# Kernel optimization log

Measured on AMD Instinct MI355X. Metric: run time of the kernel, lower is better.

## Reference

```python
import jax, jax.numpy as jnp
import numpy as np
import math

B, T, D = 2, 2048, 4096
H, HD = 32, 128  # n_head, head_dim; H*HD == D
THETA = 10000.0


def _rope_tables(T, hd, theta):
    # standard RoPE: freqs_i = theta^(-2i/hd), angle[t,i] = t * freqs_i
    inv = 1.0 / (theta ** (np.arange(0, hd, 2, dtype=np.float32) / hd))  # [hd/2]
    ang = np.arange(T, dtype=np.float32)[:, None] * inv[None, :]          # [T, hd/2]
    return jnp.asarray(np.cos(ang)), jnp.asarray(np.sin(ang))


def setup_inputs() -> dict:
    key = jax.random.key(0)
    ks = jax.random.split(key, 5)
    scale = 1.0 / math.sqrt(D)
    x = jax.random.normal(ks[0], (B, T, D), dtype=jnp.float32)
    Wq = jax.random.normal(ks[1], (D, H * HD), dtype=jnp.float32) * scale
    Wk = jax.random.normal(ks[2], (D, H * HD), dtype=jnp.float32) * scale
    Wv = jax.random.normal(ks[3], (D, H * HD), dtype=jnp.float32) * scale
    Wo = jax.random.normal(ks[4], (D, D), dtype=jnp.float32) * scale
    fc, fs = _rope_tables(T, HD, THETA)
    return {"x": x, "freqs_cos": fc, "freqs_sin": fs,
            "Wq": Wq, "Wk": Wk, "Wv": Wv, "Wo": Wo}


def _apply_rope(t, cos, sin):
    # t: [B, T, H, HD]; complex rotation on interleaved (even, odd) pairs
    tp = t.reshape(*t.shape[:-1], HD // 2, 2)
    xr, xi = tp[..., 0], tp[..., 1]
    c = cos[None, :, None, :]  # [1, T, 1, HD/2]
    s = sin[None, :, None, :]
    out_r = xr * c - xi * s
    out_i = xr * s + xi * c
    return jnp.stack([out_r, out_i], axis=-1).reshape(t.shape)


def reference(x, freqs_cos, freqs_sin, Wq, Wk, Wv, Wo):
    Bc, Tc, _ = x.shape
    q = (x @ Wq).reshape(Bc, Tc, H, HD)
    k = (x @ Wk).reshape(Bc, Tc, H, HD)
    v = (x @ Wv).reshape(Bc, Tc, H, HD)
    q = _apply_rope(q, freqs_cos, freqs_sin)
    k = _apply_rope(k, freqs_cos, freqs_sin)
    scale = 1.0 / math.sqrt(HD)
    scores = jnp.einsum('bqhd,bkhd->bhqk', q, k) * scale  # [B,H,T,T]
    causal = jnp.tril(jnp.ones((Tc, Tc), dtype=bool))
    scores = jnp.where(causal[None, None], scores, -jnp.inf)
    attn = jax.nn.softmax(scores, axis=-1)
    y = jnp.einsum('bhqk,bkhd->bqhd', attn, v).reshape(Bc, Tc, H * HD)
    return y @ Wo
```

## Files before the change

### kernel.cpp

```cpp
#include <hip/hip_runtime.h>

typedef unsigned short ushort_t;
typedef unsigned int uint32;

typedef float f32x4 __attribute__((ext_vector_type(4)));
typedef __bf16 bf16x8 __attribute__((ext_vector_type(8)));
typedef unsigned short us8 __attribute__((ext_vector_type(8)));
typedef unsigned short us4 __attribute__((ext_vector_type(4)));

#define TSEQ 2048
#define DMODEL 4096

__device__ __forceinline__ ushort_t f2bf(float f) {
  uint32 u = __builtin_bit_cast(uint32, f);
  u += 0x7FFFu + ((u >> 16) & 1u);
  return (ushort_t)(u >> 16);
}
__device__ __forceinline__ float bf2f(ushort_t u) {
  return __builtin_bit_cast(float, ((uint32)u) << 16);
}

__device__ __forceinline__ void gload_lds16(const void* g, void* l) {
  auto gp = (const __attribute__((address_space(1))) void*)g;
  auto lp = (__attribute__((address_space(3))) void*)l;
  __builtin_amdgcn_global_load_lds(gp, lp, 16, 0, 0);
}

__global__ __launch_bounds__(256) void k_cast_bf16(const float* __restrict__ in,
                                                   ushort_t* __restrict__ out, int n4) {
  int g = blockIdx.x * 256 + threadIdx.x;
  if (g >= n4) return;
  float4 v = *(const float4*)(in + (size_t)g * 4);
  us4 o; o[0] = f2bf(v.x); o[1] = f2bf(v.y); o[2] = f2bf(v.z); o[3] = f2bf(v.w);
  *(us4*)(out + (size_t)g * 4) = o;
}

__global__ __launch_bounds__(256) void k_transpose_cast(const float* __restrict__ W,
                                                        ushort_t* __restrict__ WT) {
  __shared__ __align__(16) ushort_t ts[64 * 72];
  const int tid = threadIdx.x;
  const int n0 = blockIdx.x * 64, k0 = blockIdx.y * 64;
  #pragma unroll
  for (int it = 0; it < 4; ++it) {
    int e = it * 256 + tid;
    int r = e >> 4, c4 = e & 15;
    float4 v = *(const float4*)(W + (size_t)(k0 + r) * DMODEL + n0 + c4 * 4);
    us4 o; o[0] = f2bf(v.x); o[1] = f2bf(v.y); o[2] = f2bf(v.z); o[3] = f2bf(v.w);
    *(us4*)&ts[r * 72 + c4 * 4] = o;
  }
  __syncthreads();
  #pragma unroll
  for (int it = 0; it < 4; ++it) {
    int e = it * 256 + tid;
    int r2 = e >> 4, c4 = e & 15;
    us4 o;
    #pragma unroll
    for (int j = 0; j < 4; ++j) o[j] = ts[(c4 * 4 + j) * 72 + r2];
    *(us4*)(WT + (size_t)(n0 + r2) * DMODEL + k0 + c4 * 4) = o;
  }
}

template <bool OUT_BF16>
__global__ __launch_bounds__(512, 2)
void k_gemm256(const ushort_t* __restrict__ A, const ushort_t* __restrict__ Bt,
               void* __restrict__ Cv, int M, int N, int K) {
  __shared__ __align__(16) ushort_t As[2][256 * 64];
  __shared__ __align__(16) ushort_t Bs[2][256 * 64];
  const int tid = threadIdx.x;
  const int w = tid >> 6, l = tid & 63;
  const int wr = w >> 2, wc = w & 3;
  const int lg = l >> 4, lc = l & 15;

  const int nwg = gridDim.x;
  const int cpx = nwg >> 3;
  const int wg = (blockIdx.x & 7) * cpx + (blockIdx.x >> 3);
  const int nbn = N >> 8;
  const int bm = wg / nbn, bn = wg % nbn;

  const int rowoff = l >> 3;
  const int swzck  = (l & 7) ^ rowoff;
  const ushort_t* Ab = A + (size_t)(bm * 256) * K;
  const ushort_t* Bb = Bt + (size_t)(bn * 256) * K;
  const ushort_t* gA[4]; const ushort_t* gB[4];
  int ldsOff[4];
  #pragma unroll
  for (int j = 0; j < 4; ++j) {
    int r0 = (w * 4 + j) * 8;
    gA[j] = Ab + (size_t)(r0 + rowoff) * K + swzck * 8;
    gB[j] = Bb + (size_t)(r0 + rowoff) * K + swzck * 8;
    ldsOff[j] = r0 * 64;
  }

  int offA[8][2], offB[4][2];
  #pragma unroll
  for (int m = 0; m < 8; ++m)
    #pragma unroll
    for (int kk = 0; kk < 2; ++kk)
      offA[m][kk] = (wr * 128 + m * 16 + lc) * 64 + (((kk * 4 + lg) ^ (lc & 7)) * 8);
  #pragma unroll
  for (int n = 0; n < 4; ++n)
    #pragma unroll
    for (int kk = 0; kk < 2; ++kk)
      offB[n][kk] = (wc * 64 + n * 16 + lc) * 64 + (((kk * 4 + lg) ^ (lc & 7)) * 8);

  f32x4 acc[8][4];
  #pragma unroll
  for (int m = 0; m < 8; ++m)
    #pragma unroll
    for (int n = 0; n < 4; ++n) acc[m][n] = (f32x4){0.f, 0.f, 0.f, 0.f};

  #pragma unroll
  for (int j = 0; j < 4; ++j) {
    gload_lds16(gA[j], &As[0][ldsOff[j]]);
    gload_lds16(gB[j], &Bs[0][ldsOff[j]]);
  }
  #pragma unroll
  for (int j = 0; j < 4; ++j) {
    gload_lds16(gA[j] + 64, &As[1][ldsOff[j]]);
    gload_lds16(gB[j] + 64, &Bs[1][ldsOff[j]]);
  }
  asm volatile("s_waitcnt vmcnt(8)" ::: "memory");
  __builtin_amdgcn_s_barrier();
  __builtin_amdgcn_sched_barrier(0);

  const int NT = K >> 6;
  for (int t = 0; t < NT; ++t) {
    const int cur = t & 1;
    const ushort_t* Ac = As[cur];
    const ushort_t* Bc = Bs[cur];
    bf16x8 af[4][2], bf0[2][2], bf1[2][2];

    #pragma unroll
    for (int i = 0; i < 4; ++i)
      #pragma unroll
      for (int kk = 0; kk < 2; ++kk)
        af[i][kk] = *(const bf16x8*)&Ac[offA[i][kk]];
    #pragma unroll
    for (int j2 = 0; j2 < 2; ++j2)
      #pragma unroll
      for (int kk = 0; kk < 2; ++kk)
        bf0[j2][kk] = *(const bf16x8*)&Bc[offB[j2][kk]];
    asm volatile("" ::: "memory");
    __builtin_amdgcn_s_barrier();
    __builtin_amdgcn_s_setprio(1);
    #pragma unroll
    for (int i = 0; i < 4; ++i)
      #pragma unroll
      for (int j2 = 0; j2 < 2; ++j2)
        #pragma unroll
        for (int kk = 0; kk < 2; ++kk)
          acc[i][j2] = __builtin_amdgcn_mfma_f32_16x16x32_bf16(af[i][kk], bf0[j2][kk], acc[i][j2], 0, 0, 0);
    __builtin_amdgcn_s_setprio(0);
    __builtin_amdgcn_s_barrier();
    asm volatile("" ::: "memory");

    #pragma unroll
    for (int j2 = 0; j2 < 2; ++j2)
      #pragma unroll
      for (int kk = 0; kk < 2; ++kk)
        bf1[j2][kk] = *(const bf16x8*)&Bc[offB[2 + j2][kk]];
    asm volatile("" ::: "memory");
    __builtin_amdgcn_s_barrier();
    __builtin_amdgcn_s_setprio(1);
    #pragma unroll
    for (int i = 0; i < 4; ++i)
      #pragma unroll
      for (int j2 = 0; j2 < 2; ++j2)
        #pragma unroll
        for (int kk = 0; kk < 2; ++kk)
          acc[i][2 + j2] = __builtin_amdgcn_mfma_f32_16x16x32_bf16(af[i][kk], bf1[j2][kk], acc[i][2 + j2], 0, 0, 0);
    __builtin_amdgcn_s_setprio(0);
    __builtin_amdgcn_s_barrier();
    asm volatile("" ::: "memory");

    #pragma unroll
    for (int i = 0; i < 4; ++i)
      #pragma unroll
      for (int kk = 0; kk < 2; ++kk)
        af[i][kk] = *(const bf16x8*)&Ac[offA[4 + i][kk]];
    asm volatile("" ::: "memory");
    __builtin_amdgcn_s_barrier();
    __builtin_amdgcn_s_setprio(1);
    #pragma unroll
    for (int i = 0; i < 4; ++i)
      #pragma unroll
      for (int j2 = 0; j2 < 2; ++j2)
        #pragma unroll
        for (int kk = 0; kk < 2; ++kk)
          acc[4 + i][j2] = __builtin_amdgcn_mfma_f32_16x16x32_bf16(af[i][kk], bf0[j2][kk], acc[4 + i][j2], 0, 0, 0);
    __builtin_amdgcn_s_setprio(0);
    __builtin_amdgcn_s_barrier();
    asm volatile("" ::: "memory");

    if (t + 2 < NT) {
      const int k0 = (t + 2) << 6;
      #pragma unroll
      for (int j = 0; j < 4; ++j) {
        gload_lds16(gA[j] + k0, &As[cur][ldsOff[j]]);
        gload_lds16(gB[j] + k0, &Bs[cur][ldsOff[j]]);
      }
    }
    asm volatile("" ::: "memory");
    __builtin_amdgcn_s_barrier();
    __builtin_amdgcn_s_setprio(1);
    #pragma unroll
    for (int i = 0; i < 4; ++i)
      #pragma unroll
      for (int j2 = 0; j2 < 2; ++j2)
        #pragma unroll
        for (int kk = 0; kk < 2; ++kk)
          acc[4 + i][2 + j2] = __builtin_amdgcn_mfma_f32_16x16x32_bf16(af[i][kk], bf1[j2][kk], acc[4 + i][2 + j2], 0, 0, 0);
    __builtin_amdgcn_s_setprio(0);

    if (t + 2 < NT) {
      asm volatile("s_waitcnt vmcnt(8)" ::: "memory");
    } else if (t + 1 < NT) {
      asm volatile("s_waitcnt vmcnt(0)" ::: "memory");
    }
    if (t + 1 < NT) {
      __builtin_amdgcn_s_barrier();
      __builtin_amdgcn_sched_barrier(0);
    }
  }

  #pragma unroll
  for (int m = 0; m < 8; ++m) {
    int row0 = bm * 256 + wr * 128 + m * 16 + lg * 4;
    #pragma unroll
    for (int n = 0; n < 4; ++n) {
      int col = bn * 256 + wc * 64 + n * 16 + lc;
      #pragma unroll
      for (int r = 0; r < 4; ++r) {
        float v = acc[m][n][r];
        if (OUT_BF16) ((ushort_t*)Cv)[(size_t)(row0 + r) * N + col] = f2bf(v);
        else          ((float*)Cv)[(size_t)(row0 + r) * N + col] = v;
      }
    }
  }
}

__global__ __launch_bounds__(256) void k_rope(ushort_t* __restrict__ q, ushort_t* __restrict__ k,
                                              const float* __restrict__ fc,
                                              const float* __restrict__ fs) {
  int g = blockIdx.x * 256 + threadIdx.x;
  size_t base = (size_t)g * 8;
  int row = (int)(base >> 12);
  int col = (int)(base & 4095);
  int t = row & (TSEQ - 1);
  int i0 = (col & 127) >> 1;
  float4 c = *(const float4*)(fc + t * 64 + i0);
  float4 s = *(const float4*)(fs + t * 64 + i0);
  ushort_t* bufs[2] = {q, k};
  #pragma unroll
  for (int bi = 0; bi < 2; ++bi) {
    us8 v = *(const us8*)(bufs[bi] + base);
    us8 o;
    float xr, xi;
    xr = bf2f(v[0]); xi = bf2f(v[1]);
    o[0] = f2bf(xr * c.x - xi * s.x); o[1] = f2bf(xr * s.x + xi * c.x);
    xr = bf2f(v[2]); xi = bf2f(v[3]);
    o[2] = f2bf(xr * c.y - xi * s.y); o[3] = f2bf(xr * s.y + xi * c.y);
    xr = bf2f(v[4]); xi = bf2f(v[5]);
    o[4] = f2bf(xr * c.z - xi * s.z); o[5] = f2bf(xr * s.z + xi * c.z);
    xr = bf2f(v[6]); xi = bf2f(v[7]);
    o[6] = f2bf(xr * c.w - xi * s.w); o[7] = f2bf(xr * s.w + xi * c.w);
    *(us8*)(bufs[bi] + base) = o;
  }
}

__global__ __launch_bounds__(512, 2)
void k_attn(const ushort_t* __restrict__ Q, const ushort_t* __restrict__ Kb,
            const ushort_t* __restrict__ Vt, ushort_t* __restrict__ Y) {
  __shared__ __align__(16) ushort_t Ks[64 * 128];
  __shared__ __align__(16) ushort_t Vs[128 * 64];
  __shared__ __align__(16) ushort_t Ps[8][16 * 64];
  const int bx = blockIdx.x, h = blockIdx.y, b = blockIdx.z;
  const int tid = threadIdx.x;
  const int w = tid >> 6, l = tid & 63;
  const int lg = l >> 4, lc = l & 15;
  const float scale = 0.08838834764831845f;
  const float THR = 8.0f;

  for (int qi = 0; qi < 2; ++qi) {
    const int qt = qi ? (15 - bx) : bx;
    const int q0 = qt * 128;
    const int wrow0 = q0 + w * 16;

    bf16x8 qf[4];
    {
      const ushort_t* qp = Q + (size_t)(b * TSEQ + wrow0 + lc) * DMODEL + h * 128;
      #pragma unroll
      for (int ks = 0; ks < 4; ++ks) qf[ks] = *(const bf16x8*)(qp + ks * 32 + lg * 8);
    }

    float m_r[4], lp[4];
    #pragma unroll
    for (int r = 0; r < 4; ++r) { m_r[r] = -1e30f; lp[r] = 0.f; }
    f32x4 o[8];
    #pragma unroll
    for (int t = 0; t < 8; ++t) o[t] = (f32x4){0.f, 0.f, 0.f, 0.f};

    const int nkv = (qt + 1) * 2;
    for (int kt = 0; kt < nkv; ++kt) {
      const int kv0 = kt * 64;
      #pragma unroll
      for (int i = 0; i < 2; ++i) {
        int cdx = tid + i * 512;
        int row = cdx >> 4, ch = cdx & 15;
        us8 v = *(const us8*)(Kb + (size_t)(b * TSEQ + kv0 + row) * DMODEL + h * 128 + ch * 8);
        *(us8*)&Ks[row * 128 + ((ch * 8) ^ ((row & 7) * 8))] = v;
      }
      #pragma unroll
      for (int i = 0; i < 2; ++i) {
        int cdx = tid + i * 512;
        int row = cdx >> 3, ch = cdx & 7;
        us8 v = *(const us8*)(Vt + (size_t)(h * 128 + row) * DMODEL + b * TSEQ + kv0 + ch * 8);
        *(us8*)&Vs[row * 64 + ((ch * 8) ^ ((row & 7) * 8))] = v;
      }
      __syncthreads();

      if (kv0 <= wrow0 + 15) {
        f32x4 s[4];
        __builtin_amdgcn_s_setprio(1);
        #pragma unroll
        for (int n = 0; n < 4; ++n) {
          s[n] = (f32x4){0.f, 0.f, 0.f, 0.f};
          #pragma unroll
          for (int ks = 0; ks < 4; ++ks) {
            int row = n * 16 + lc;
            bf16x8 kf = *(const bf16x8*)&Ks[row * 128 + ((ks * 32 + lg * 8) ^ ((row & 7) * 8))];
            s[n] = __builtin_amdgcn_mfma_f32_16x16x32_bf16(qf[ks], kf, s[n], 0, 0, 0);
          }
        }
        __builtin_amdgcn_s_setprio(0);

        float sv[4][4];
        if (kv0 + 63 > wrow0) {
          #pragma unroll
          for (int n = 0; n < 4; ++n)
            #pragma unroll
            for (int r = 0; r < 4; ++r) {
              float x = s[n][r] * scale;
              int kvg = kv0 + n * 16 + lc;
              int qg = wrow0 + lg * 4 + r;
              sv[n][r] = (kvg > qg) ? -1e30f : x;
            }
        } else {
          #pragma unroll
          for (int n = 0; n < 4; ++n)
            #pragma unroll
            for (int r = 0; r < 4; ++r) sv[n][r] = s[n][r] * scale;
        }

        float pmax[4];
        #pragma unroll
        for (int r = 0; r < 4; ++r)
          pmax[r] = fmaxf(fmaxf(sv[0][r], sv[1][r]), fmaxf(sv[2][r], sv[3][r]));
        bool ok = (pmax[0] <= m_r[0] + THR) && (pmax[1] <= m_r[1] + THR) &&
                  (pmax[2] <= m_r[2] + THR) && (pmax[3] <= m_r[3] + THR);
        if (!__all(ok)) {
          #pragma unroll
          for (int r = 0; r < 4; ++r) {
            float mx = pmax[r];
            #pragma unroll
            for (int off = 1; off < 16; off <<= 1) mx = fmaxf(mx, __shfl_xor(mx, off, 16));
            float mn = fmaxf(m_r[r], mx);
            float al = __expf(m_r[r] - mn);
            m_r[r] = mn;
            lp[r] *= al;
            #pragma unroll
            for (int t = 0; t < 8; ++t) o[t][r] *= al;
          }
        }

        #pragma unroll
        for (int n = 0; n < 4; ++n)
          #pragma unroll
          for (int r = 0; r < 4; ++r) {
            float p = __expf(sv[n][r] - m_r[r]);
            lp[r] += p;
            int row = lg * 4 + r, col = n * 16 + lc;
            Ps[w][row * 64 + (col ^ ((row & 7) * 8))] = f2bf(p);
          }

        __builtin_amdgcn_s_setprio(1);
        #pragma unroll
        for (int kvs = 0; kvs < 2; ++kvs) {
          bf16x8 pa = *(const bf16x8*)&Ps[w][lc * 64 + ((kvs * 32 + lg * 8) ^ ((lc & 7) * 8))];
          #pragma unroll
          for (int t = 0; t < 8; ++t) {
            int vrow = t * 16 + lc;
            bf16x8 vb = *(const bf16x8*)&Vs[vrow * 64 + ((kvs * 32 + lg * 8) ^ ((vrow & 7) * 8))];
            o[t] = __builtin_amdgcn_mfma_f32_16x16x32_bf16(pa, vb, o[t], 0, 0, 0);
          }
        }
        __builtin_amdgcn_s_setprio(0);
      }
      __syncthreads();
    }

    float linv[4];
    #pragma unroll
    for (int r = 0; r < 4; ++r) {
      float ls = lp[r];
      #pragma unroll
      for (int off = 1; off < 16; off <<= 1) ls += __shfl_xor(ls, off, 16);
      linv[r] = 1.0f / ls;
    }

    #pragma unroll
    for (int t = 0; t < 8; ++t)
      #pragma unroll
      for (int r = 0; r < 4; ++r) {
        int row = wrow0 + lg * 4 + r;
        int col = h * 128 + t * 16 + lc;
        Y[(size_t)(b * TSEQ + row) * DMODEL + col] = f2bf(o[t][r] * linv[r]);
      }
  }
}

extern "C" void kernel_launch(void* const* d_in, const int* in_sizes, int n_in,
                              void* d_out, int out_size, void* d_ws, size_t ws_size,
                              hipStream_t stream) {
  const float* x  = (const float*)d_in[0];
  const float* fc = (const float*)d_in[1];
  const float* fs = (const float*)d_in[2];
  const float* Wq = (const float*)d_in[3];
  const float* Wk = (const float*)d_in[4];
  const float* Wv = (const float*)d_in[5];
  const float* Wo = (const float*)d_in[6];

  const size_t SZ = (size_t)4096 * 4096;
  ushort_t* xb  = (ushort_t*)d_ws;
  ushort_t* WqT = xb + SZ;
  ushort_t* WkT = WqT + SZ;
  ushort_t* WvT = WkT + SZ;
  ushort_t* WoT = WvT + SZ;
  ushort_t* qb  = WoT + SZ;
  ushort_t* kb  = qb + SZ;
  ushort_t* vT  = kb + SZ;
  ushort_t* yb  = vT + SZ;

  k_cast_bf16<<<16384, 256, 0, stream>>>(x, xb, 4194304);
  dim3 tg(64, 64);
  k_transpose_cast<<<tg, 256, 0, stream>>>(Wq, WqT);
  k_transpose_cast<<<tg, 256, 0, stream>>>(Wk, WkT);
  k_transpose_cast<<<tg, 256, 0, stream>>>(Wv, WvT);
  k_transpose_cast<<<tg, 256, 0, stream>>>(Wo, WoT);

  k_gemm256<true><<<256, 512, 0, stream>>>(xb, WqT, qb, 4096, 4096, 4096);
  k_gemm256<true><<<256, 512, 0, stream>>>(xb, WkT, kb, 4096, 4096, 4096);
  k_gemm256<true><<<256, 512, 0, stream>>>(WvT, xb, vT, 4096, 4096, 4096);

  k_rope<<<8192, 256, 0, stream>>>(qb, kb, fc, fs);

  dim3 ag(8, 32, 2);
  k_attn<<<ag, 512, 0, stream>>>(qb, kb, vT, yb);

  k_gemm256<false><<<256, 512, 0, stream>>>(yb, WoT, d_out, 4096, 4096, 4096);
}
```

Before: 954.4 us.

## Double-buffer K/V tiles with async global-to-LDS loads in attention

The attention kernel now keeps two K/V tile buffers in shared memory and fills the next one with direct global-to-LDS loads while the current tile is being computed. It waits with explicit vmcnt counters and raw barriers instead of a full __syncthreads on every iteration. The launch becomes a 1D grid that maps blocks so the same (b,h) group stays on one XCD for L2 locality, and the P swizzle pattern changes. The cost is doubled LDS use, which may limit occupancy, and correctness now depends on hand-tuned waitcnt values.

```diff
diff --git a/kernel.cpp b/kernel.cpp
--- a/kernel.cpp
+++ b/kernel.cpp
@@ -271,16 +271,39 @@
 __global__ __launch_bounds__(512, 2)
 void k_attn(const ushort_t* __restrict__ Q, const ushort_t* __restrict__ Kb,
             const ushort_t* __restrict__ Vt, ushort_t* __restrict__ Y) {
-  __shared__ __align__(16) ushort_t Ks[64 * 128];
-  __shared__ __align__(16) ushort_t Vs[128 * 64];
+  __shared__ __align__(16) ushort_t Ks[2][64 * 128];
+  __shared__ __align__(16) ushort_t Vs[2][128 * 64];
   __shared__ __align__(16) ushort_t Ps[8][16 * 64];
-  const int bx = blockIdx.x, h = blockIdx.y, b = blockIdx.z;
+  const int id = blockIdx.x;
+  const int xcd = id & 7, slot = id >> 3;
+  const int bx = slot & 7, gHi = slot >> 3;
+  const int g = gHi * 8 + xcd;
+  const int h = g & 31, b = g >> 5;
   const int tid = threadIdx.x;
   const int w = tid >> 6, l = tid & 63;
   const int lg = l >> 4, lc = l & 15;
   const float scale = 0.08838834764831845f;
   const float THR = 8.0f;
 
+  auto stageKV = [&](int kv0, int buf) {
+    #pragma unroll
+    for (int i = 0; i < 2; ++i) {
+      int seg = w * 2 + i;
+      {
+        int row = seg * 4 + (l >> 4);
+        int csrc = (l & 15) ^ (row & 7);
+        gload_lds16(Kb + (size_t)(b * TSEQ + kv0 + row) * DMODEL + h * 128 + csrc * 8,
+                    &Ks[buf][seg * 512]);
+      }
+      {
+        int row = seg * 8 + (l >> 3);
+        int csrc = (l & 7) ^ (l >> 3);
+        gload_lds16(Vt + (size_t)(h * 128 + row) * DMODEL + b * TSEQ + kv0 + csrc * 8,
+                    &Vs[buf][seg * 512]);
+      }
+    }
+  };
+
   for (int qi = 0; qi < 2; ++qi) {
     const int qt = qi ? (15 - bx) : bx;
     const int q0 = qt * 128;
@@ -301,23 +324,17 @@
     for (int t = 0; t < 8; ++t) o[t] = (f32x4){0.f, 0.f, 0.f, 0.f};
 
     const int nkv = (qt + 1) * 2;
+    stageKV(0, 0);
     for (int kt = 0; kt < nkv; ++kt) {
+      const int cur = kt & 1;
       const int kv0 = kt * 64;
-      #pragma unroll
-      for (int i = 0; i < 2; ++i) {
-        int cdx = tid + i * 512;
-        int row = cdx >> 4, ch = cdx & 15;
-        us8 v = *(const us8*)(Kb + (size_t)(b * TSEQ + kv0 + row) * DMODEL + h * 128 + ch * 8);
-        *(us8*)&Ks[row * 128 + ((ch * 8) ^ ((row & 7) * 8))] = v;
-      }
-      #pragma unroll
-      for (int i = 0; i < 2; ++i) {
-        int cdx = tid + i * 512;
-        int row = cdx >> 3, ch = cdx & 7;
-        us8 v = *(const us8*)(Vt + (size_t)(h * 128 + row) * DMODEL + b * TSEQ + kv0 + ch * 8);
-        *(us8*)&Vs[row * 64 + ((ch * 8) ^ ((row & 7) * 8))] = v;
-      }
-      __syncthreads();
+      if (kt + 1 < nkv) {
+        stageKV((kt + 1) * 64, cur ^ 1);
+        asm volatile("s_waitcnt vmcnt(4)" ::: "memory");
+      } else {
+        asm volatile("s_waitcnt vmcnt(0)" ::: "memory");
+      }
+      __builtin_amdgcn_s_barrier();
 
       if (kv0 <= wrow0 + 15) {
         f32x4 s[4];
@@ -328,7 +345,7 @@
           #pragma unroll
           for (int ks = 0; ks < 4; ++ks) {
             int row = n * 16 + lc;
-            bf16x8 kf = *(const bf16x8*)&Ks[row * 128 + ((ks * 32 + lg * 8) ^ ((row & 7) * 8))];
+            bf16x8 kf = *(const bf16x8*)&Ks[cur][row * 128 + ((ks * 32 + lg * 8) ^ ((row & 7) * 8))];
             s[n] = __builtin_amdgcn_mfma_f32_16x16x32_bf16(qf[ks], kf, s[n], 0, 0, 0);
           }
         }
@@ -380,23 +397,24 @@
             float p = __expf(sv[n][r] - m_r[r]);
             lp[r] += p;
             int row = lg * 4 + r, col = n * 16 + lc;
-            Ps[w][row * 64 + (col ^ ((row & 7) * 8))] = f2bf(p);
+            Ps[w][row * 64 + (col ^ (lg * 16))] = f2bf(p);
           }
 
         __builtin_amdgcn_s_setprio(1);
         #pragma unroll
         for (int kvs = 0; kvs < 2; ++kvs) {
-          bf16x8 pa = *(const bf16x8*)&Ps[w][lc * 64 + ((kvs * 32 + lg * 8) ^ ((lc & 7) * 8))];
+          bf16x8 pa = *(const bf16x8*)&Ps[w][lc * 64 + ((kvs * 32 + lg * 8) ^ ((lc >> 2) * 16))];
           #pragma unroll
           for (int t = 0; t < 8; ++t) {
             int vrow = t * 16 + lc;
-            bf16x8 vb = *(const bf16x8*)&Vs[vrow * 64 + ((kvs * 32 + lg * 8) ^ ((vrow & 7) * 8))];
+            bf16x8 vb = *(const bf16x8*)&Vs[cur][vrow * 64 + ((kvs * 32 + lg * 8) ^ ((vrow & 7) * 8))];
             o[t] = __builtin_amdgcn_mfma_f32_16x16x32_bf16(pa, vb, o[t], 0, 0, 0);
           }
         }
         __builtin_amdgcn_s_setprio(0);
       }
-      __syncthreads();
+      asm volatile("" ::: "memory");
+      __builtin_amdgcn_s_barrier();
     }
 
     float linv[4];
@@ -454,8 +472,7 @@
 
   k_rope<<<8192, 256, 0, stream>>>(qb, kb, fc, fs);
 
-  dim3 ag(8, 32, 2);
-  k_attn<<<ag, 512, 0, stream>>>(qb, kb, vT, yb);
+  k_attn<<<512, 512, 0, stream>>>(qb, kb, vT, yb);
 
   k_gemm256<false><<<256, 512, 0, stream>>>(yb, WoT, d_out, 4096, 4096, 4096);
 }
```

Result: faster. 887.7 us (-7.0%).
